# Kernel optimization log

Hardware: AMD Instinct MI355X
Metric: run time of the kernel (lower is better)

Reference implementation:

```python
import jax, jax.numpy as jnp
import numpy as np

B, Ng, C, H, W, Nt, M, P = 4, 8192, 256, 128, 128, 512, 8, 4
Ch = C // M  # 32 channels per head
EPS = 1e-5


def setup_inputs():
    key = jax.random.key(0)
    ks = jax.random.split(key, 12)
    s = 0.02
    def w(k, shape):
        return jax.random.normal(k, shape, jnp.float32) * s
    return {
        "query": jax.random.normal(ks[0], (B, Ng, C), jnp.float32),
        "value": jax.random.normal(ks[1], (B, C, H, W), jnp.float32),
        "reference_points": jax.random.uniform(ks[2], (B, Ng, 2), dtype=jnp.float32),
        "trajectory_points": jax.random.uniform(ks[3], (B, Nt, 2), dtype=jnp.float32),
        "in_proj_w": w(ks[4], (3 * C, C)),
        "in_proj_b": jnp.zeros((3 * C,), jnp.float32),
        "mha_out_w": w(ks[5], (C, C)),
        "mha_out_b": jnp.zeros((C,), jnp.float32),
        "ln_g": jnp.ones((C,), jnp.float32),
        "ln_b": jnp.zeros((C,), jnp.float32),
        "traj_w": w(ks[6], (C, 2)),
        "traj_b": jnp.zeros((C,), jnp.float32),
        "offs_w": w(ks[7], (M * P * 2, C)),
        "offs_b": jnp.zeros((M * P * 2,), jnp.float32),
        "attw_w": w(ks[8], (M * P, C)),
        "attw_b": jnp.zeros((M * P,), jnp.float32),
        "out_w": w(ks[9], (C, C)),
        "out_b": jnp.zeros((C,), jnp.float32),
    }


def _bilinear_sample(imgf, x, y):
    # imgf: (NM, Ch, H*W); x, y: (NM, Lq, P) unnormalized pixel coords
    # grid_sample semantics: bilinear, padding_mode='zeros', align_corners=False
    NM = imgf.shape[0]
    Lq, Pp = x.shape[1], x.shape[2]
    x0 = jnp.floor(x); y0 = jnp.floor(y)
    x1 = x0 + 1.0;     y1 = y0 + 1.0

    def gather(xi, yi):
        valid = (xi >= 0) & (xi < W) & (yi >= 0) & (yi < H)
        xc = jnp.clip(xi, 0, W - 1).astype(jnp.int32)
        yc = jnp.clip(yi, 0, H - 1).astype(jnp.int32)
        idx = (yc * W + xc).reshape(NM, 1, Lq * Pp)
        v = jnp.take_along_axis(imgf, jnp.broadcast_to(idx, (NM, Ch, Lq * Pp)), axis=2)
        return v.reshape(NM, Ch, Lq, Pp), valid.astype(imgf.dtype)

    v00, m00 = gather(x0, y0)
    v01, m01 = gather(x1, y0)
    v10, m10 = gather(x0, y1)
    v11, m11 = gather(x1, y1)
    wx1 = x - x0; wx0 = 1.0 - wx1
    wy1 = y - y0; wy0 = 1.0 - wy1
    out = (v00 * (wx0 * wy0 * m00)[:, None]
         + v01 * (wx1 * wy0 * m01)[:, None]
         + v10 * (wx0 * wy1 * m10)[:, None]
         + v11 * (wx1 * wy1 * m11)[:, None])
    return out  # (NM, Ch, Lq, P)


def reference(query, value, reference_points, trajectory_points,
              in_proj_w, in_proj_b, mha_out_w, mha_out_b, ln_g, ln_b,
              traj_w, traj_b, offs_w, offs_b, attw_w, attw_b, out_w, out_b):
    # trajectory projection: (B,Nt,2) -> (B,Nt,C)
    tf = trajectory_points @ traj_w.T + traj_b

    # guidance cross-attention (nn.MultiheadAttention, eval mode => no dropout)
    wq, wk, wv = jnp.split(in_proj_w, 3, axis=0)
    bq, bk, bv = jnp.split(in_proj_b, 3, axis=0)
    q = (query @ wq.T + bq).reshape(B, Ng, M, Ch)
    k = (tf @ wk.T + bk).reshape(B, Nt, M, Ch)
    v = (tf @ wv.T + bv).reshape(B, Nt, M, Ch)
    scores = jnp.einsum('bqmc,bkmc->bmqk', q, k) / jnp.sqrt(jnp.float32(Ch))
    probs = jax.nn.softmax(scores, axis=-1)
    ctx = jnp.einsum('bmqk,bkmc->bqmc', probs, v).reshape(B, Ng, C)
    ctx = ctx @ mha_out_w.T + mha_out_b

    # residual + LayerNorm
    x = query + ctx
    mu = x.mean(-1, keepdims=True)
    var = ((x - mu) ** 2).mean(-1, keepdims=True)
    gq = (x - mu) / jnp.sqrt(var + EPS) * ln_g + ln_b

    # sampling offsets & softmax attention weights (L=1 level)
    offs = (gq @ offs_w.T + offs_b).reshape(B, Ng, M, 1, P, 2)
    aw = jax.nn.softmax((gq @ attw_w.T + attw_b).reshape(B, Ng, M, P), axis=-1)
    loc = reference_points[:, :, None, None, None, :] + offs  # (B,Ng,M,1,P,2)

    # deformable sampling core (single level)
    grid = 2.0 * loc[:, :, :, 0] - 1.0                   # (B,Ng,M,P,2)
    grid = grid.transpose(0, 2, 1, 3, 4).reshape(B * M, Ng, P, 2)
    gx = (grid[..., 0] + 1.0) * (W * 0.5) - 0.5
    gy = (grid[..., 1] + 1.0) * (H * 0.5) - 0.5
    imgf = value.reshape(B * M, Ch, H * W)               # per-head feature maps
    samp = _bilinear_sample(imgf, gx, gy)                # (B*M,Ch,Ng,P)
    w_att = aw.transpose(0, 2, 1, 3).reshape(B * M, 1, Ng, P)
    out = (samp * w_att).sum(-1)                         # (B*M,Ch,Ng)

    # faithful to source: view(B,M,Ch,Ng).transpose(1,2).contiguous().view(B,Ng,C)
    out = out.reshape(B, M, Ch, Ng).transpose(0, 2, 1, 3).reshape(B, Ng, C)
    return out @ out_w.T + out_b
```

## Files before the change

kernel.cpp:

```cpp
#include <hip/hip_runtime.h>
#include <hip/hip_bf16.h>
#include <stdint.h>

typedef __bf16 bf16_t;
typedef __bf16 bf16x8 __attribute__((ext_vector_type(8)));
typedef __bf16 bf16x4 __attribute__((ext_vector_type(4)));
typedef float f32x4 __attribute__((ext_vector_type(4)));

#define CEXP 0.25506807186679906f

__device__ __forceinline__ float ldf(const void* p, size_t i, int isf) {
  return isf ? ((const float*)p)[i] : (float)((const bf16_t*)p)[i];
}

__device__ __forceinline__ int detect_isf(const void* q) {
  const uint16_t* u = (const uint16_t*)q;
  const int lane = threadIdx.x & 63;
  const uint16_t v = u[2 * lane];
  const int e = (v >> 7) & 0xFF;
  const int weird = (e >= 0x86 || (v != 0 && e <= 0x65)) ? 1 : 0;
  return (__popcll(__ballot(weird)) >= 16) ? 1 : 0;
}

__device__ __forceinline__ float fexp2(float x) {
#if __has_builtin(__builtin_amdgcn_exp2f)
  return __builtin_amdgcn_exp2f(x);
#else
  return exp2f(x);
#endif
}

__device__ __forceinline__ f32x4 mfma16x16x16(bf16x4 a, bf16x4 b, f32x4 c) {
#if __has_builtin(__builtin_amdgcn_mfma_f32_16x16x16_bf16)
  return __builtin_amdgcn_mfma_f32_16x16x16_bf16(a, b, c, 0, 0, 0);
#else
  typedef short s16x4 __attribute__((ext_vector_type(4)));
  return __builtin_amdgcn_mfma_f32_16x16x16bf16_1k(
      __builtin_bit_cast(s16x4, a), __builtin_bit_cast(s16x4, b), c, 0, 0, 0);
#endif
}

__device__ __forceinline__ void stage16(const bf16_t* g, bf16_t* l) {
  __builtin_amdgcn_global_load_lds((const __attribute__((address_space(1))) void*)g,
                                   (__attribute__((address_space(3))) void*)l, 16, 0, 0);
}

__global__ __launch_bounds__(256) void prep_all(
    const void* __restrict__ query,
    const void* in_w, const void* in_b, const void* mow, const void* mob,
    const void* outw, const void* outb,
    const void* trajp, const void* tw, const void* tb,
    const void* offs_w, const void* attw_w, const void* offs_b, const void* attw_b,
    bf16_t* __restrict__ blob, bf16_t* __restrict__ tf,
    bf16_t* __restrict__ Wph, bf16_t* __restrict__ Wpl, bf16_t* __restrict__ bp)
{
  const int isf = detect_isf(query);
  const int bid = blockIdx.x;
  if (bid < 322) {
    const int g = (bid * 256 + threadIdx.x) * 4;
    if (g >= 328960) return;
    const void* src; size_t off;
    if      (g < 196608) { src = in_w; off = g; }
    else if (g < 197376) { src = in_b; off = g - 196608; }
    else if (g < 262912) { src = mow;  off = g - 197376; }
    else if (g < 263168) { src = mob;  off = g - 262912; }
    else if (g < 328704) { src = outw; off = g - 263168; }
    else                 { src = outb; off = g - 328704; }
#pragma unroll
    for (int k = 0; k < 4; k++) blob[g + k] = (bf16_t)ldf(src, off + k, isf);
  } else if (bid < 322 + 2048) {
    const int rowb = bid - 322;
    const int c = threadIdx.x;
    const float x = ldf(trajp, rowb * 2 + 0, isf);
    const float y = ldf(trajp, rowb * 2 + 1, isf);
    const float v = x * ldf(tw, c * 2 + 0, isf) + y * ldf(tw, c * 2 + 1, isf) + ldf(tb, c, isf);
    tf[(size_t)rowb * 256 + c] = (bf16_t)v;
  } else {
    const int idx = (bid - 2370) * 256 + threadIdx.x;
    const int rowp = idx >> 8, c = idx & 255;
    float v = 0.0f;
    if (rowp < 64)      v = ldf(offs_w, rowp * 256 + c, isf);
    else if (rowp < 96) v = ldf(attw_w, (rowp - 64) * 256 + c, isf);
    const bf16_t hi = (bf16_t)v;
    Wph[idx] = hi;
    Wpl[idx] = (bf16_t)(v - (float)hi);
    if (idx < 128) {
      float bv = 0.0f;
      if (idx < 64)      bv = ldf(offs_b, idx, isf);
      else if (idx < 96) bv = ldf(attw_b, idx - 64, isf);
      bp[idx] = (bf16_t)bv;
    }
  }
}

#define TM 128
#define TN 128
#define TKK 64

__global__ __launch_bounds__(256) void gemm_async(
    const bf16_t* __restrict__ A, const bf16_t* __restrict__ W,
    const bf16_t* __restrict__ bias, void* __restrict__ Cout,
    void* __restrict__ Cout2, int Ndim, int Kdim, int mode, float kscale,
    const void* __restrict__ qdet)
{
  __shared__ __align__(16) bf16_t As[TM * TKK];
  __shared__ __align__(16) bf16_t Ws[TN * TKK];
  const int t    = threadIdx.x;
  const int lane = t & 63;
  const int w    = t >> 6;
  const int wm   = (w & 1) * 64;
  const int wn   = (w >> 1) * 64;
  const int q4   = lane >> 4;
  const int r16  = lane & 15;
  const int tm   = blockIdx.x * TM;
  const int tn   = blockIdx.y * TN;

  f32x4 acc[4][4] = {};

  for (int kt = 0; kt < Kdim; kt += TKK) {
    __syncthreads();
#pragma unroll
    for (int r = 0; r < 4; r++) {
      const int L = w * 256 + r * 64 + lane;
      const int R = L >> 3, c = (L & 7) * 8;
      stage16(A + (size_t)(tm + R) * Kdim + kt + c, As + L * 8);
      stage16(W + (size_t)(tn + R) * Kdim + kt + c, Ws + L * 8);
    }
    __syncthreads();
#pragma unroll
    for (int ks = 0; ks < TKK; ks += 32) {
      bf16x8 af[4], bfm[4];
#pragma unroll
      for (int i = 0; i < 4; i++)
        af[i] = *(const bf16x8*)(As + (wm + 16 * i + r16) * TKK + ks + q4 * 8);
#pragma unroll
      for (int j = 0; j < 4; j++)
        bfm[j] = *(const bf16x8*)(Ws + (wn + 16 * j + r16) * TKK + ks + q4 * 8);
#pragma unroll
      for (int i = 0; i < 4; i++)
#pragma unroll
        for (int j = 0; j < 4; j++)
          acc[i][j] = __builtin_amdgcn_mfma_f32_16x16x32_bf16(af[i], bfm[j], acc[i][j], 0, 0, 0);
    }
  }

  const int isf = (mode == 3) ? detect_isf(qdet) : 1;
#pragma unroll
  for (int j = 0; j < 4; j++) {
    const int col = tn + wn + 16 * j + r16;
    const float bv = (float)bias[col];
#pragma unroll
    for (int i = 0; i < 4; i++) {
      const int row0 = tm + wm + 16 * i + q4 * 4;
#pragma unroll
      for (int rr = 0; rr < 4; rr++) {
        const float v = acc[i][j][rr] + bv;
        const size_t off = (size_t)(row0 + rr) * Ndim + col;
        if (mode == 0) {
          ((bf16_t*)Cout)[off] = (bf16_t)v;
        } else if (mode == 6) {
          const int rowg = row0 + rr;
          if (col < 256) {
            ((bf16_t*)Cout)[(size_t)rowg * 256 + col] = (bf16_t)(v * kscale);
          } else {
            const int bb = rowg >> 9, tt = rowg & 511;
            const int c2 = col - 256;
            const int mm = c2 >> 5, ch = c2 & 31;
            ((bf16_t*)Cout2)[(((size_t)(bb * 8 + mm) * 32 + ch) << 9) + tt] = (bf16_t)v;
          }
        } else {
          if (isf) ((float*)Cout)[off] = v; else ((bf16_t*)Cout)[off] = (bf16_t)v;
        }
      }
    }
  }
}

__global__ __launch_bounds__(256) void gemm_f32a(
    const void* __restrict__ Araw, const bf16_t* __restrict__ W,
    const bf16_t* __restrict__ bias, bf16_t* __restrict__ Cout,
    int Ndim, int Kdim, const void* __restrict__ qdet)
{
  __shared__ __align__(16) bf16_t As[TM * TKK];
  __shared__ __align__(16) bf16_t Ws[TN * TKK];
  const int t    = threadIdx.x;
  const int lane = t & 63;
  const int w    = t >> 6;
  const int wm   = (w & 1) * 64;
  const int wn   = (w >> 1) * 64;
  const int q4   = lane >> 4;
  const int r16  = lane & 15;
  const int tm   = blockIdx.x * TM;
  const int tn   = blockIdx.y * TN;
  const int aisf = detect_isf(qdet);

  f32x4 acc[4][4] = {};
  const int srow = t >> 1;
  const int skb  = (t & 1) * 32;

  for (int kt = 0; kt < Kdim; kt += TKK) {
    __syncthreads();
    if (aisf) {
      const float4* ga = (const float4*)((const float*)Araw + (size_t)(tm + srow) * Kdim + kt + skb);
#pragma unroll
      for (int kk = 0; kk < 8; kk++) {
        const float4 u = ga[kk];
        bf16x4 h = {(bf16_t)u.x, (bf16_t)u.y, (bf16_t)u.z, (bf16_t)u.w};
        *(bf16x4*)(As + srow * TKK + skb + kk * 4) = h;
      }
    } else {
      const uint4* ga = (const uint4*)((const bf16_t*)Araw + (size_t)(tm + srow) * Kdim + kt + skb);
      uint4* la = (uint4*)(As + srow * TKK + skb);
      la[0] = ga[0]; la[1] = ga[1]; la[2] = ga[2]; la[3] = ga[3];
    }
    {
      const uint4* gw = (const uint4*)(W + (size_t)(tn + srow) * Kdim + kt + skb);
      uint4* lw = (uint4*)(Ws + srow * TKK + skb);
      lw[0] = gw[0]; lw[1] = gw[1]; lw[2] = gw[2]; lw[3] = gw[3];
    }
    __syncthreads();
#pragma unroll
    for (int ks = 0; ks < TKK; ks += 32) {
      bf16x8 af[4], bfm[4];
#pragma unroll
      for (int i = 0; i < 4; i++)
        af[i] = *(const bf16x8*)(As + (wm + 16 * i + r16) * TKK + ks + q4 * 8);
#pragma unroll
      for (int j = 0; j < 4; j++)
        bfm[j] = *(const bf16x8*)(Ws + (wn + 16 * j + r16) * TKK + ks + q4 * 8);
#pragma unroll
      for (int i = 0; i < 4; i++)
#pragma unroll
        for (int j = 0; j < 4; j++)
          acc[i][j] = __builtin_amdgcn_mfma_f32_16x16x32_bf16(af[i], bfm[j], acc[i][j], 0, 0, 0);
    }
  }

#pragma unroll
  for (int j = 0; j < 4; j++) {
    const int col = tn + wn + 16 * j + r16;
    const float bv = (float)bias[col];
#pragma unroll
    for (int i = 0; i < 4; i++) {
      const int row0 = tm + wm + 16 * i + q4 * 4;
#pragma unroll
      for (int rr = 0; rr < 4; rr++)
        Cout[(size_t)(row0 + rr) * Ndim + col] = (bf16_t)(acc[i][j][rr] + bv);
    }
  }
}

__global__ __launch_bounds__(256, 2) void attn_kernel(
    const bf16_t* __restrict__ Q, const bf16_t* __restrict__ Kk,
    const bf16_t* __restrict__ Vt, bf16_t* __restrict__ ctx)
{
  const int t = threadIdx.x;
  const int lane = t & 63, w = t >> 6;
  const int q4 = lane >> 4, r16 = lane & 15;
  const int bm = blockIdx.y;
  const int b = bm >> 3, m = bm & 7;
  const int q0 = blockIdx.x * 512 + w * 128;

  bf16x8 qf[8];
#pragma unroll
  for (int qt = 0; qt < 8; qt++)
    qf[qt] = *(const bf16x8*)(Q + ((size_t)(b * 8192 + q0 + qt * 16 + r16) * 256 + m * 32 + q4 * 8));

  f32x4 acc[8][2] = {};
  float lsum[8] = {0.f, 0.f, 0.f, 0.f, 0.f, 0.f, 0.f, 0.f};

  const bf16_t* kbase  = Kk + (size_t)b * 512 * 256 + m * 32 + (size_t)r16 * 256 + q4 * 8;
  const bf16_t* vbase0 = Vt + (size_t)bm * 32 * 512 + ((size_t)r16 << 9) + q4 * 4;
  const bf16_t* vbase1 = vbase0 + (16 << 9);

  bf16x8 kfA = *(const bf16x8*)(kbase);
  bf16x4 v0A = *(const bf16x4*)(vbase0);
  bf16x4 v1A = *(const bf16x4*)(vbase1);
  bf16x8 kfB = *(const bf16x8*)(kbase + (size_t)16 * 256);
  bf16x4 v0B = *(const bf16x4*)(vbase0 + 16);
  bf16x4 v1B = *(const bf16x4*)(vbase1 + 16);

  for (int k0 = 0; k0 < 512; k0 += 32) {
    const bf16x8 ka = kfA;
    const bf16x4 va0 = v0A, va1 = v1A;
    kfA = *(const bf16x8*)(kbase + (size_t)(k0 + 32) * 256);
    v0A = *(const bf16x4*)(vbase0 + k0 + 32);
    v1A = *(const bf16x4*)(vbase1 + k0 + 32);
    __builtin_amdgcn_s_setprio(1);
#pragma unroll
    for (int qt = 0; qt < 8; qt++) {
      f32x4 z = {};
      const f32x4 s = __builtin_amdgcn_mfma_f32_16x16x32_bf16(ka, qf[qt], z, 0, 0, 0);
      const float e0 = fexp2(s[0]), e1 = fexp2(s[1]);
      const float e2 = fexp2(s[2]), e3 = fexp2(s[3]);
      lsum[qt] += (e0 + e1) + (e2 + e3);
      const bf16x4 p = {(bf16_t)e0, (bf16_t)e1, (bf16_t)e2, (bf16_t)e3};
      acc[qt][0] = mfma16x16x16(va0, p, acc[qt][0]);
      acc[qt][1] = mfma16x16x16(va1, p, acc[qt][1]);
    }
    __builtin_amdgcn_s_setprio(0);
    const bf16x8 kb = kfB;
    const bf16x4 vb0 = v0B, vb1 = v1B;
    kfB = *(const bf16x8*)(kbase + (size_t)(k0 + 48) * 256);
    v0B = *(const bf16x4*)(vbase0 + k0 + 48);
    v1B = *(const bf16x4*)(vbase1 + k0 + 48);
    __builtin_amdgcn_s_setprio(1);
#pragma unroll
    for (int qt = 0; qt < 8; qt++) {
      f32x4 z = {};
      const f32x4 s = __builtin_amdgcn_mfma_f32_16x16x32_bf16(kb, qf[qt], z, 0, 0, 0);
      const float e0 = fexp2(s[0]), e1 = fexp2(s[1]);
      const float e2 = fexp2(s[2]), e3 = fexp2(s[3]);
      lsum[qt] += (e0 + e1) + (e2 + e3);
      const bf16x4 p = {(bf16_t)e0, (bf16_t)e1, (bf16_t)e2, (bf16_t)e3};
      acc[qt][0] = mfma16x16x16(vb0, p, acc[qt][0]);
      acc[qt][1] = mfma16x16x16(vb1, p, acc[qt][1]);
    }
    __builtin_amdgcn_s_setprio(0);
  }

#pragma unroll
  for (int qt = 0; qt < 8; qt++) {
    float v = lsum[qt];
    v += __shfl_xor(v, 16, 64);
    v += __shfl_xor(v, 32, 64);
    const float inv = 1.0f / v;
    const size_t row = (size_t)b * 8192 + q0 + qt * 16 + r16;
    bf16x4 o0, o1;
#pragma unroll
    for (int rr = 0; rr < 4; rr++) {
      o0[rr] = (bf16_t)(acc[qt][0][rr] * inv);
      o1[rr] = (bf16_t)(acc[qt][1][rr] * inv);
    }
    *(bf16x4*)(ctx + row * 256 + m * 32 + q4 * 4)      = o0;
    *(bf16x4*)(ctx + row * 256 + m * 32 + 16 + q4 * 4) = o1;
  }
}

__global__ __launch_bounds__(256) void ln_kernel(
    const bf16_t* __restrict__ y2, const void* __restrict__ query,
    const void* __restrict__ g, const void* __restrict__ beta,
    bf16_t* __restrict__ gqh, bf16_t* __restrict__ gql)
{
  const int isf = detect_isf(query);
  const int rowb = blockIdx.x * 4 + (threadIdx.x >> 6);
  const int lane = threadIdx.x & 63;
  const size_t base = (size_t)rowb * 256;
  const int c0 = lane * 4;
  float x[4];
  {
    const bf16x4 yv = *(const bf16x4*)(y2 + base + c0);
    if (isf) {
      const float4 qv = *(const float4*)((const float*)query + base + c0);
      x[0] = qv.x + (float)yv[0]; x[1] = qv.y + (float)yv[1];
      x[2] = qv.z + (float)yv[2]; x[3] = qv.w + (float)yv[3];
    } else {
      const bf16x4 qv = *(const bf16x4*)((const bf16_t*)query + base + c0);
#pragma unroll
      for (int k = 0; k < 4; k++) x[k] = (float)qv[k] + (float)yv[k];
    }
  }
  float s = x[0] + x[1] + x[2] + x[3];
  for (int d = 1; d < 64; d <<= 1) s += __shfl_xor(s, d, 64);
  const float mu = s * (1.0f / 256.0f);
  float vs = 0.f;
#pragma unroll
  for (int k = 0; k < 4; k++) { const float d = x[k] - mu; vs += d * d; }
  for (int d = 1; d < 64; d <<= 1) vs += __shfl_xor(vs, d, 64);
  const float rstd = rsqrtf(vs * (1.0f / 256.0f) + 1e-5f);
  float gw[4], bb[4];
  if (isf) {
    const float4 gg = *(const float4*)((const float*)g + c0);
    const float4 bv = *(const float4*)((const float*)beta + c0);
    gw[0] = gg.x; gw[1] = gg.y; gw[2] = gg.z; gw[3] = gg.w;
    bb[0] = bv.x; bb[1] = bv.y; bb[2] = bv.z; bb[3] = bv.w;
  } else {
    const bf16x4 gg = *(const bf16x4*)((const bf16_t*)g + c0);
    const bf16x4 bv = *(const bf16x4*)((const bf16_t*)beta + c0);
#pragma unroll
    for (int k = 0; k < 4; k++) { gw[k] = (float)gg[k]; bb[k] = (float)bv[k]; }
  }
  bf16x4 hi4, lo4;
#pragma unroll
  for (int k = 0; k < 4; k++) {
    const float gv = (x[k] - mu) * rstd * gw[k] + bb[k];
    const bf16_t hi = (bf16_t)gv;
    hi4[k] = hi;
    lo4[k] = (bf16_t)(gv - (float)hi);
  }
  *(bf16x4*)(gqh + base + c0) = hi4;
  *(bf16x4*)(gql + base + c0) = lo4;
}

__global__ __launch_bounds__(256) void gemm_offs(
    const bf16_t* __restrict__ Ahg, const bf16_t* __restrict__ Alg,
    const bf16_t* __restrict__ Whg, const bf16_t* __restrict__ Wlg,
    const bf16_t* __restrict__ bias, float* __restrict__ Cout)
{
  __shared__ __align__(16) bf16_t Ah[128 * 64];
  __shared__ __align__(16) bf16_t Al[128 * 64];
  __shared__ __align__(16) bf16_t Wh[128 * 64];
  __shared__ __align__(16) bf16_t Wl[128 * 64];
  const int t    = threadIdx.x;
  const int lane = t & 63;
  const int w    = t >> 6;
  const int wm   = (w & 1) * 64;
  const int wn   = (w >> 1) * 64;
  const int q4   = lane >> 4;
  const int r16  = lane & 15;
  const int tm   = blockIdx.x * 128;

  f32x4 acc[4][4] = {};
  const int srow = t >> 1;
  const int skb  = (t & 1) * 32;

  for (int kt = 0; kt < 256; kt += 64) {
    __syncthreads();
    {
      const uint4* g0 = (const uint4*)(Ahg + (size_t)(tm + srow) * 256 + kt + skb);
      uint4* l0 = (uint4*)(Ah + srow * 64 + skb);
      l0[0] = g0[0]; l0[1] = g0[1]; l0[2] = g0[2]; l0[3] = g0[3];
      const uint4* g1 = (const uint4*)(Alg + (size_t)(tm + srow) * 256 + kt + skb);
      uint4* l1 = (uint4*)(Al + srow * 64 + skb);
      l1[0] = g1[0]; l1[1] = g1[1]; l1[2] = g1[2]; l1[3] = g1[3];
      const uint4* g2 = (const uint4*)(Whg + (size_t)srow * 256 + kt + skb);
      uint4* l2 = (uint4*)(Wh + srow * 64 + skb);
      l2[0] = g2[0]; l2[1] = g2[1]; l2[2] = g2[2]; l2[3] = g2[3];
      const uint4* g3 = (const uint4*)(Wlg + (size_t)srow * 256 + kt + skb);
      uint4* l3 = (uint4*)(Wl + srow * 64 + skb);
      l3[0] = g3[0]; l3[1] = g3[1]; l3[2] = g3[2]; l3[3] = g3[3];
    }
    __syncthreads();
#pragma unroll
    for (int ks = 0; ks < 64; ks += 32) {
      bf16x8 ah[4], al[4], bh[4], bl[4];
#pragma unroll
      for (int i = 0; i < 4; i++) {
        ah[i] = *(const bf16x8*)(Ah + (wm + 16 * i + r16) * 64 + ks + q4 * 8);
        al[i] = *(const bf16x8*)(Al + (wm + 16 * i + r16) * 64 + ks + q4 * 8);
      }
#pragma unroll
      for (int j = 0; j < 4; j++) {
        bh[j] = *(const bf16x8*)(Wh + (wn + 16 * j + r16) * 64 + ks + q4 * 8);
        bl[j] = *(const bf16x8*)(Wl + (wn + 16 * j + r16) * 64 + ks + q4 * 8);
      }
#pragma unroll
      for (int i = 0; i < 4; i++)
#pragma unroll
        for (int j = 0; j < 4; j++) {
          f32x4 a = acc[i][j];
          a = __builtin_amdgcn_mfma_f32_16x16x32_bf16(al[i], bh[j], a, 0, 0, 0);
          a = __builtin_amdgcn_mfma_f32_16x16x32_bf16(ah[i], bl[j], a, 0, 0, 0);
          a = __builtin_amdgcn_mfma_f32_16x16x32_bf16(ah[i], bh[j], a, 0, 0, 0);
          acc[i][j] = a;
        }
    }
  }

#pragma unroll
  for (int j = 0; j < 4; j++) {
    const int col = wn + 16 * j + r16;
    const float bv = (float)bias[col];
    const int live  = (col < 96) ? 1 : 0;
    const int moff  = (col < 64) ? (col >> 3) : ((col - 64) >> 2);
    const int inner = (col < 64) ? (col & 7) : (8 + (col & 3));
#pragma unroll
    for (int i = 0; i < 4; i++) {
      const int row0 = tm + wm + 16 * i + q4 * 4;
#pragma unroll
      for (int rr = 0; rr < 4; rr++) {
        if (live) {
          const int row = row0 + rr;
          const int bq = row >> 13, q = row & 8191;
          Cout[(((size_t)(bq * 8 + moff) << 13) + q) * 16 + inner] = acc[i][j][rr] + bv;
        }
      }
    }
  }
}

__global__ __launch_bounds__(256) void transpose_value(
    const void* __restrict__ V, bf16_t* __restrict__ Vp, const void* __restrict__ qdet)
{
  __shared__ __align__(16) bf16_t tile[32][136];
  const int isf = detect_isf(qdet);
  const int bid = blockIdx.x;
  const int h = bid & 127;
  const int bm = bid >> 7;
  const int b = bm >> 3, mm = bm & 7;
  const int t = threadIdx.x;
  const int ch  = t >> 3;
  const int ww0 = (t & 7) * 16;
  const size_t ibase = (((size_t)b * 256 + mm * 32 + ch) * 128 + h) * 128 + ww0;
  if (isf) {
    const float4* src = (const float4*)((const float*)V + ibase);
    bf16x8 h0, h1;
#pragma unroll
    for (int k = 0; k < 2; k++) {
      const float4 u0 = src[k * 2], u1 = src[k * 2 + 1];
      bf16x8 hh = {(bf16_t)u0.x, (bf16_t)u0.y, (bf16_t)u0.z, (bf16_t)u0.w,
                   (bf16_t)u1.x, (bf16_t)u1.y, (bf16_t)u1.z, (bf16_t)u1.w};
      if (k == 0) h0 = hh; else h1 = hh;
    }
    *(bf16x8*)(&tile[ch][ww0])     = h0;
    *(bf16x8*)(&tile[ch][ww0 + 8]) = h1;
  } else {
    const bf16x8* src = (const bf16x8*)((const bf16_t*)V + ibase);
    *(bf16x8*)(&tile[ch][ww0])     = src[0];
    *(bf16x8*)(&tile[ch][ww0 + 8]) = src[1];
  }
  __syncthreads();
  const size_t base = ((size_t)bm * 128 + h) * 4096;
  const int ww = t >> 1;
  const int c0 = (t & 1) * 16;
  bf16x8 o0, o1;
#pragma unroll
  for (int e = 0; e < 8; e++) { o0[e] = tile[c0 + e][ww]; o1[e] = tile[c0 + 8 + e][ww]; }
  *(bf16x8*)(Vp + base + ww * 32 + c0)     = o0;
  *(bf16x8*)(Vp + base + ww * 32 + c0 + 8) = o1;
}

__global__ __launch_bounds__(256) void sampler(
    const float* __restrict__ ys2, const void* __restrict__ refp,
    const bf16_t* __restrict__ vperm, bf16_t* __restrict__ outs,
    const void* __restrict__ qdet)
{
  const int isf = detect_isf(qdet);
  const int t = threadIdx.x;
  const int wg = blockIdx.x;
  const int bm  = (wg & 7) + ((wg >> 9) << 3);
  const int mid = (wg >> 3) & 63;
  const int qt  = mid >> 1;
  const int hf  = mid & 1;
  const int b = bm >> 3, m = bm & 7;
  const int qq = qt * 256 + t;
  const size_t row = (size_t)b * 8192 + qq;
  const float* y16 = ys2 + (((size_t)bm << 13) + qq) * 16;
  const float rx = ldf(refp, row * 2 + 0, isf);
  const float ry = ldf(refp, row * 2 + 1, isf);

  const float4 off01 = *(const float4*)(y16 + 0);
  const float4 off23 = *(const float4*)(y16 + 4);
  const float4 lg    = *(const float4*)(y16 + 8);

  const float mx = fmaxf(fmaxf(lg.x, lg.y), fmaxf(lg.z, lg.w));
  const float e0 = __expf(lg.x - mx), e1 = __expf(lg.y - mx);
  const float e2 = __expf(lg.z - mx), e3 = __expf(lg.w - mx);
  const float inv = 1.0f / (e0 + e1 + e2 + e3);
  const float aw[4] = {e0 * inv, e1 * inv, e2 * inv, e3 * inv};
  const float ox[4] = {off01.x, off01.z, off23.x, off23.z};
  const float oy[4] = {off01.y, off01.w, off23.y, off23.w};

  float acc[16];
#pragma unroll
  for (int ch = 0; ch < 16; ch++) acc[ch] = 0.0f;

  const bf16_t* vbase = vperm + (size_t)bm * (128 * 128 * 32) + hf * 16;

  for (int p = 0; p < 4; p++) {
    const float gx = (rx + ox[p]) * 128.0f - 0.5f;
    const float gy = (ry + oy[p]) * 128.0f - 0.5f;
    const float x0f = floorf(gx), y0f = floorf(gy);
    const int x0 = (int)x0f, y0i = (int)y0f;
    const float wx1 = gx - x0f, wx0 = 1.0f - wx1;
    const float wy1 = gy - y0f, wy0 = 1.0f - wy1;
    const float a = aw[p];
    for (int cy = 0; cy < 2; cy++) {
      const int yy = y0i + cy;
      if (yy < 0 || yy >= 128) continue;
      const float wy = cy ? wy1 : wy0;
      for (int cx = 0; cx < 2; cx++) {
        const int xx = x0 + cx;
        if (xx < 0 || xx >= 128) continue;
        const float wgt = a * wy * (cx ? wx1 : wx0);
        const bf16x8* src8 = (const bf16x8*)(vbase + ((size_t)yy * 128 + xx) * 32);
        const bf16x8 d0 = src8[0];
        const bf16x8 d1 = src8[1];
#pragma unroll
        for (int e = 0; e < 8; e++) {
          acc[e]     += wgt * (float)d0[e];
          acc[8 + e] += wgt * (float)d1[e];
        }
      }
    }
  }

  const size_t obase = (size_t)b * 8192;
#pragma unroll
  for (int ch = 0; ch < 16; ch++) {
    const int chg = hf * 16 + ch;
    const size_t orow = obase + (size_t)(chg * 8 + m) * 32 + qt;
    outs[orow * 256 + t] = (bf16_t)acc[ch];
  }
}

extern "C" void kernel_launch(void* const* d_in, const int* in_sizes, int n_in,
                              void* d_out, int out_size, void* d_ws, size_t ws_size,
                              hipStream_t stream) {
  const void* query = d_in[0];
  const void* value = d_in[1];
  const void* refp  = d_in[2];
  const void* trajp = d_in[3];
  const void* in_w  = d_in[4];
  const void* in_b  = d_in[5];
  const void* mow   = d_in[6];
  const void* mob   = d_in[7];
  const void* lng   = d_in[8];
  const void* lnb   = d_in[9];
  const void* tw    = d_in[10];
  const void* tb    = d_in[11];
  const void* ow    = d_in[12];
  const void* ob    = d_in[13];
  const void* aww   = d_in[14];
  const void* awb   = d_in[15];
  const void* outw  = d_in[16];
  const void* outb  = d_in[17];

  char* base = (char*)d_ws;
  float*  ysamp = (float*)(base);
  bf16_t* qout  = (bf16_t*)(base + 16777216);
  bf16_t* ctx   = (bf16_t*)(base + 33554432);
  bf16_t* y2    = (bf16_t*)(base + 50331648);
  bf16_t* tf_ws = (bf16_t*)(base + 67108864);
  bf16_t* k_ws  = (bf16_t*)(base + 68157440);
  bf16_t* vt_g  = (bf16_t*)(base + 69206016);
  bf16_t* blob  = (bf16_t*)(base + 70254592);

  bf16_t* gqh   = qout;
  bf16_t* gql   = ctx;
  bf16_t* vperm = (bf16_t*)(base + 16777216);
  bf16_t* outs  = y2;

  bf16_t* inw_bf  = blob;
  bf16_t* inb_bf  = blob + 196608;
  bf16_t* mow_bf  = blob + 197376;
  bf16_t* mob_bf  = blob + 262912;
  bf16_t* outw_bf = blob + 263168;
  bf16_t* outb_bf = blob + 328704;
  bf16_t* wph     = blob + 328960;
  bf16_t* wpl     = blob + 361728;
  bf16_t* bpad    = blob + 394496;

  prep_all<<<dim3(2498), dim3(256), 0, stream>>>(
      query, in_w, in_b, mow, mob, outw, outb, trajp, tw, tb,
      ow, aww, ob, awb, blob, tf_ws, wph, wpl, bpad);
  gemm_async<<<dim3(16, 4), dim3(256), 0, stream>>>(
      tf_ws, inw_bf + 65536, inb_bf + 256, (void*)k_ws, (void*)vt_g, 512, 256, 6, CEXP, query);
  gemm_f32a<<<dim3(256, 2), dim3(256), 0, stream>>>(
      query, inw_bf, inb_bf, qout, 256, 256, query);
  attn_kernel<<<dim3(16, 32), dim3(256), 0, stream>>>(qout, k_ws, vt_g, ctx);
  gemm_async<<<dim3(256, 2), dim3(256), 0, stream>>>(
      ctx, mow_bf, mob_bf, (void*)y2, nullptr, 256, 256, 0, 1.0f, query);
  ln_kernel<<<dim3(8192), dim3(256), 0, stream>>>(y2, query, lng, lnb, gqh, gql);
  gemm_offs<<<dim3(256, 1), dim3(256), 0, stream>>>(gqh, gql, wph, wpl, bpad, ysamp);
  transpose_value<<<dim3(4096), dim3(256), 0, stream>>>(value, vperm, query);
  sampler<<<dim3(2048), dim3(256), 0, stream>>>(ysamp, refp, vperm, outs, query);
  gemm_async<<<dim3(256, 2), dim3(256), 0, stream>>>(
      outs, outw_bf, outb_bf, d_out, nullptr, 256, 256, 3, 1.0f, query);
}
```

Measured before the change: 336.3 us.

## Fuse value transpose into prep kernel and merge Q and KV projections

Moves the value-tensor transpose/bf16 conversion out of its own launch and into the prep_all kernel as extra blocks. Vperm gets its own workspace region so it no longer aliases qout. The separate Q projection and K/V projection GEMMs become one gemm_qkv launch that dispatches on block index. This removes two kernel launches and lets independent work share one grid, at the cost of a larger prep grid and a bigger workspace footprint.

```diff
diff --git a/kernel.cpp b/kernel.cpp
--- a/kernel.cpp
+++ b/kernel.cpp
@@ -52,8 +52,10 @@
     const void* trajp, const void* tw, const void* tb,
     const void* offs_w, const void* attw_w, const void* offs_b, const void* attw_b,
     bf16_t* __restrict__ blob, bf16_t* __restrict__ tf,
-    bf16_t* __restrict__ Wph, bf16_t* __restrict__ Wpl, bf16_t* __restrict__ bp)
+    bf16_t* __restrict__ Wph, bf16_t* __restrict__ Wpl, bf16_t* __restrict__ bp,
+    const void* __restrict__ V, bf16_t* __restrict__ Vp)
 {
+  __shared__ __align__(16) bf16_t tile[32][136];
   const int isf = detect_isf(query);
   const int bid = blockIdx.x;
   if (bid < 322) {
@@ -75,7 +77,7 @@
     const float y = ldf(trajp, rowb * 2 + 1, isf);
     const float v = x * ldf(tw, c * 2 + 0, isf) + y * ldf(tw, c * 2 + 1, isf) + ldf(tb, c, isf);
     tf[(size_t)rowb * 256 + c] = (bf16_t)v;
-  } else {
+  } else if (bid < 2498) {
     const int idx = (bid - 2370) * 256 + threadIdx.x;
     const int rowp = idx >> 8, c = idx & 255;
     float v = 0.0f;
@@ -90,6 +92,41 @@
       else if (idx < 96) bv = ldf(attw_b, idx - 64, isf);
       bp[idx] = (bf16_t)bv;
     }
+  } else {
+    const int vb = bid - 2498;
+    const int h = vb & 127;
+    const int bm = vb >> 7;
+    const int b = bm >> 3, mm = bm & 7;
+    const int t = threadIdx.x;
+    const int ch  = t >> 3;
+    const int ww0 = (t & 7) * 16;
+    const size_t ibase = (((size_t)b * 256 + mm * 32 + ch) * 128 + h) * 128 + ww0;
+    if (isf) {
+      const float4* src = (const float4*)((const float*)V + ibase);
+      bf16x8 h0, h1;
+#pragma unroll
+      for (int k = 0; k < 2; k++) {
+        const float4 u0 = src[k * 2], u1 = src[k * 2 + 1];
+        bf16x8 hh = {(bf16_t)u0.x, (bf16_t)u0.y, (bf16_t)u0.z, (bf16_t)u0.w,
+                     (bf16_t)u1.x, (bf16_t)u1.y, (bf16_t)u1.z, (bf16_t)u1.w};
+        if (k == 0) h0 = hh; else h1 = hh;
+      }
+      *(bf16x8*)(&tile[ch][ww0])     = h0;
+      *(bf16x8*)(&tile[ch][ww0 + 8]) = h1;
+    } else {
+      const bf16x8* src = (const bf16x8*)((const bf16_t*)V + ibase);
+      *(bf16x8*)(&tile[ch][ww0])     = src[0];
+      *(bf16x8*)(&tile[ch][ww0 + 8]) = src[1];
+    }
+    __syncthreads();
+    const size_t base = ((size_t)bm * 128 + h) * 4096;
+    const int ww = t >> 1;
+    const int c0 = (t & 1) * 16;
+    bf16x8 o0, o1;
+#pragma unroll
+    for (int e = 0; e < 8; e++) { o0[e] = tile[c0 + e][ww]; o1[e] = tile[c0 + 8 + e][ww]; }
+    *(bf16x8*)(Vp + base + ww * 32 + c0)     = o0;
+    *(bf16x8*)(Vp + base + ww * 32 + c0 + 8) = o1;
   }
 }
 
@@ -158,16 +195,6 @@
         const size_t off = (size_t)(row0 + rr) * Ndim + col;
         if (mode == 0) {
           ((bf16_t*)Cout)[off] = (bf16_t)v;
-        } else if (mode == 6) {
-          const int rowg = row0 + rr;
-          if (col < 256) {
-            ((bf16_t*)Cout)[(size_t)rowg * 256 + col] = (bf16_t)(v * kscale);
-          } else {
-            const int bb = rowg >> 9, tt = rowg & 511;
-            const int c2 = col - 256;
-            const int mm = c2 >> 5, ch = c2 & 31;
-            ((bf16_t*)Cout2)[(((size_t)(bb * 8 + mm) * 32 + ch) << 9) + tt] = (bf16_t)v;
-          }
         } else {
           if (isf) ((float*)Cout)[off] = v; else ((bf16_t*)Cout)[off] = (bf16_t)v;
         }
@@ -176,10 +203,12 @@
   }
 }
 
-__global__ __launch_bounds__(256) void gemm_f32a(
-    const void* __restrict__ Araw, const bf16_t* __restrict__ W,
-    const bf16_t* __restrict__ bias, bf16_t* __restrict__ Cout,
-    int Ndim, int Kdim, const void* __restrict__ qdet)
+__global__ __launch_bounds__(256) void gemm_qkv(
+    const void* __restrict__ Araw, const bf16_t* __restrict__ Wq,
+    const bf16_t* __restrict__ bq, bf16_t* __restrict__ Cq,
+    const bf16_t* __restrict__ Atf, const bf16_t* __restrict__ Wkv,
+    const bf16_t* __restrict__ bkv, bf16_t* __restrict__ Kout,
+    bf16_t* __restrict__ Vtout, float kscale, const void* __restrict__ qdet)
 {
   __shared__ __align__(16) bf16_t As[TM * TKK];
   __shared__ __align__(16) bf16_t Ws[TN * TKK];
@@ -190,62 +219,120 @@
   const int wn   = (w >> 1) * 64;
   const int q4   = lane >> 4;
   const int r16  = lane & 15;
-  const int tm   = blockIdx.x * TM;
-  const int tn   = blockIdx.y * TN;
-  const int aisf = detect_isf(qdet);
+  const int blk  = blockIdx.x;
 
   f32x4 acc[4][4] = {};
-  const int srow = t >> 1;
-  const int skb  = (t & 1) * 32;
-
-  for (int kt = 0; kt < Kdim; kt += TKK) {
-    __syncthreads();
-    if (aisf) {
-      const float4* ga = (const float4*)((const float*)Araw + (size_t)(tm + srow) * Kdim + kt + skb);
-#pragma unroll
-      for (int kk = 0; kk < 8; kk++) {
-        const float4 u = ga[kk];
-        bf16x4 h = {(bf16_t)u.x, (bf16_t)u.y, (bf16_t)u.z, (bf16_t)u.w};
-        *(bf16x4*)(As + srow * TKK + skb + kk * 4) = h;
-      }
-    } else {
-      const uint4* ga = (const uint4*)((const bf16_t*)Araw + (size_t)(tm + srow) * Kdim + kt + skb);
-      uint4* la = (uint4*)(As + srow * TKK + skb);
-      la[0] = ga[0]; la[1] = ga[1]; la[2] = ga[2]; la[3] = ga[3];
-    }
-    {
-      const uint4* gw = (const uint4*)(W + (size_t)(tn + srow) * Kdim + kt + skb);
-      uint4* lw = (uint4*)(Ws + srow * TKK + skb);
-      lw[0] = gw[0]; lw[1] = gw[1]; lw[2] = gw[2]; lw[3] = gw[3];
-    }
-    __syncthreads();
-#pragma unroll
-    for (int ks = 0; ks < TKK; ks += 32) {
-      bf16x8 af[4], bfm[4];
-#pragma unroll
-      for (int i = 0; i < 4; i++)
-        af[i] = *(const bf16x8*)(As + (wm + 16 * i + r16) * TKK + ks + q4 * 8);
-#pragma unroll
-      for (int j = 0; j < 4; j++)
-        bfm[j] = *(const bf16x8*)(Ws + (wn + 16 * j + r16) * TKK + ks + q4 * 8);
-#pragma unroll
-      for (int i = 0; i < 4; i++)
+
+  if (blk < 512) {
+    const int tm = (blk >> 1) * TM;
+    const int tn = (blk & 1) * TN;
+    const int aisf = detect_isf(qdet);
+    const int srow = t >> 1;
+    const int skb  = (t & 1) * 32;
+
+    for (int kt = 0; kt < 256; kt += TKK) {
+      __syncthreads();
+      if (aisf) {
+        const float4* ga = (const float4*)((const float*)Araw + (size_t)(tm + srow) * 256 + kt + skb);
+#pragma unroll
+        for (int kk = 0; kk < 8; kk++) {
+          const float4 u = ga[kk];
+          bf16x4 h = {(bf16_t)u.x, (bf16_t)u.y, (bf16_t)u.z, (bf16_t)u.w};
+          *(bf16x4*)(As + srow * TKK + skb + kk * 4) = h;
+        }
+      } else {
+        const uint4* ga = (const uint4*)((const bf16_t*)Araw + (size_t)(tm + srow) * 256 + kt + skb);
+        uint4* la = (uint4*)(As + srow * TKK + skb);
+        la[0] = ga[0]; la[1] = ga[1]; la[2] = ga[2]; la[3] = ga[3];
+      }
+      {
+        const uint4* gw = (const uint4*)(Wq + (size_t)(tn + srow) * 256 + kt + skb);
+        uint4* lw = (uint4*)(Ws + srow * TKK + skb);
+        lw[0] = gw[0]; lw[1] = gw[1]; lw[2] = gw[2]; lw[3] = gw[3];
+      }
+      __syncthreads();
+#pragma unroll
+      for (int ks = 0; ks < TKK; ks += 32) {
+        bf16x8 af[4], bfm[4];
+#pragma unroll
+        for (int i = 0; i < 4; i++)
+          af[i] = *(const bf16x8*)(As + (wm + 16 * i + r16) * TKK + ks + q4 * 8);
 #pragma unroll
         for (int j = 0; j < 4; j++)
-          acc[i][j] = __builtin_amdgcn_mfma_f32_16x16x32_bf16(af[i], bfm[j], acc[i][j], 0, 0, 0);
-    }
-  }
-
-#pragma unroll
-  for (int j = 0; j < 4; j++) {
-    const int col = tn + wn + 16 * j + r16;
-    const float bv = (float)bias[col];
-#pragma unroll
-    for (int i = 0; i < 4; i++) {
-      const int row0 = tm + wm + 16 * i + q4 * 4;
-#pragma unroll
-      for (int rr = 0; rr < 4; rr++)
-        Cout[(size_t)(row0 + rr) * Ndim + col] = (bf16_t)(acc[i][j][rr] + bv);
+          bfm[j] = *(const bf16x8*)(Ws + (wn + 16 * j + r16) * TKK + ks + q4 * 8);
+#pragma unroll
+        for (int i = 0; i < 4; i++)
+#pragma unroll
+          for (int j = 0; j < 4; j++)
+            acc[i][j] = __builtin_amdgcn_mfma_f32_16x16x32_bf16(af[i], bfm[j], acc[i][j], 0, 0, 0);
+      }
+    }
+
+#pragma unroll
+    for (int j = 0; j < 4; j++) {
+      const int col = tn + wn + 16 * j + r16;
+      const float bv = (float)bq[col];
+#pragma unroll
+      for (int i = 0; i < 4; i++) {
+        const int row0 = tm + wm + 16 * i + q4 * 4;
+#pragma unroll
+        for (int rr = 0; rr < 4; rr++)
+          Cq[(size_t)(row0 + rr) * 256 + col] = (bf16_t)(acc[i][j][rr] + bv);
+      }
+    }
+  } else {
+    const int k = blk - 512;
+    const int tm = (k & 15) * TM;
+    const int tn = (k >> 4) * TN;
+
+    for (int kt = 0; kt < 256; kt += TKK) {
+      __syncthreads();
+#pragma unroll
+      for (int r = 0; r < 4; r++) {
+        const int L = w * 256 + r * 64 + lane;
+        const int R = L >> 3, c = (L & 7) * 8;
+        stage16(Atf + (size_t)(tm + R) * 256 + kt + c, As + L * 8);
+        stage16(Wkv + (size_t)(tn + R) * 256 + kt + c, Ws + L * 8);
+      }
+      __syncthreads();
+#pragma unroll
+      for (int ks = 0; ks < TKK; ks += 32) {
+        bf16x8 af[4], bfm[4];
+#pragma unroll
+        for (int i = 0; i < 4; i++)
+          af[i] = *(const bf16x8*)(As + (wm + 16 * i + r16) * TKK + ks + q4 * 8);
+#pragma unroll
+        for (int j = 0; j < 4; j++)
+          bfm[j] = *(const bf16x8*)(Ws + (wn + 16 * j + r16) * TKK + ks + q4 * 8);
+#pragma unroll
+        for (int i = 0; i < 4; i++)
+#pragma unroll
+          for (int j = 0; j < 4; j++)
+            acc[i][j] = __builtin_amdgcn_mfma_f32_16x16x32_bf16(af[i], bfm[j], acc[i][j], 0, 0, 0);
+      }
+    }
+
+#pragma unroll
+    for (int j = 0; j < 4; j++) {
+      const int col = tn + wn + 16 * j + r16;
+      const float bv = (float)bkv[col];
+#pragma unroll
+      for (int i = 0; i < 4; i++) {
+        const int row0 = tm + wm + 16 * i + q4 * 4;
+#pragma unroll
+        for (int rr = 0; rr < 4; rr++) {
+          const float v = acc[i][j][rr] + bv;
+          const int rowg = row0 + rr;
+          if (col < 256) {
+            Kout[(size_t)rowg * 256 + col] = (bf16_t)(v * kscale);
+          } else {
+            const int bb = rowg >> 9, tt = rowg & 511;
+            const int c2 = col - 256;
+            const int mm = c2 >> 5, ch = c2 & 31;
+            Vtout[(((size_t)(bb * 8 + mm) * 32 + ch) << 9) + tt] = (bf16_t)v;
+          }
+        }
+      }
     }
   }
 }
@@ -477,47 +564,6 @@
       }
     }
   }
-}
-
-__global__ __launch_bounds__(256) void transpose_value(
-    const void* __restrict__ V, bf16_t* __restrict__ Vp, const void* __restrict__ qdet)
-{
-  __shared__ __align__(16) bf16_t tile[32][136];
-  const int isf = detect_isf(qdet);
-  const int bid = blockIdx.x;
-  const int h = bid & 127;
-  const int bm = bid >> 7;
-  const int b = bm >> 3, mm = bm & 7;
-  const int t = threadIdx.x;
-  const int ch  = t >> 3;
-  const int ww0 = (t & 7) * 16;
-  const size_t ibase = (((size_t)b * 256 + mm * 32 + ch) * 128 + h) * 128 + ww0;
-  if (isf) {
-    const float4* src = (const float4*)((const float*)V + ibase);
-    bf16x8 h0, h1;
-#pragma unroll
-    for (int k = 0; k < 2; k++) {
-      const float4 u0 = src[k * 2], u1 = src[k * 2 + 1];
-      bf16x8 hh = {(bf16_t)u0.x, (bf16_t)u0.y, (bf16_t)u0.z, (bf16_t)u0.w,
-                   (bf16_t)u1.x, (bf16_t)u1.y, (bf16_t)u1.z, (bf16_t)u1.w};
-      if (k == 0) h0 = hh; else h1 = hh;
-    }
-    *(bf16x8*)(&tile[ch][ww0])     = h0;
-    *(bf16x8*)(&tile[ch][ww0 + 8]) = h1;
-  } else {
-    const bf16x8* src = (const bf16x8*)((const bf16_t*)V + ibase);
-    *(bf16x8*)(&tile[ch][ww0])     = src[0];
-    *(bf16x8*)(&tile[ch][ww0 + 8]) = src[1];
-  }
-  __syncthreads();
-  const size_t base = ((size_t)bm * 128 + h) * 4096;
-  const int ww = t >> 1;
-  const int c0 = (t & 1) * 16;
-  bf16x8 o0, o1;
-#pragma unroll
-  for (int e = 0; e < 8; e++) { o0[e] = tile[c0 + e][ww]; o1[e] = tile[c0 + 8 + e][ww]; }
-  *(bf16x8*)(Vp + base + ww * 32 + c0)     = o0;
-  *(bf16x8*)(Vp + base + ww * 32 + c0 + 8) = o1;
 }
 
 __global__ __launch_bounds__(256) void sampler(
@@ -628,7 +674,7 @@
 
   bf16_t* gqh   = qout;
   bf16_t* gql   = ctx;
-  bf16_t* vperm = (bf16_t*)(base + 16777216);
+  bf16_t* vperm = (bf16_t*)(base + 134217728);
   bf16_t* outs  = y2;
 
   bf16_t* inw_bf  = blob;
@@ -641,19 +687,17 @@
   bf16_t* wpl     = blob + 361728;
   bf16_t* bpad    = blob + 394496;
 
-  prep_all<<<dim3(2498), dim3(256), 0, stream>>>(
+  prep_all<<<dim3(6594), dim3(256), 0, stream>>>(
       query, in_w, in_b, mow, mob, outw, outb, trajp, tw, tb,
-      ow, aww, ob, awb, blob, tf_ws, wph, wpl, bpad);
-  gemm_async<<<dim3(16, 4), dim3(256), 0, stream>>>(
-      tf_ws, inw_bf + 65536, inb_bf + 256, (void*)k_ws, (void*)vt_g, 512, 256, 6, CEXP, query);
-  gemm_f32a<<<dim3(256, 2), dim3(256), 0, stream>>>(
-      query, inw_bf, inb_bf, qout, 256, 256, query);
+      ow, aww, ob, awb, blob, tf_ws, wph, wpl, bpad, value, vperm);
+  gemm_qkv<<<dim3(576), dim3(256), 0, stream>>>(
+      query, inw_bf, inb_bf, qout,
+      tf_ws, inw_bf + 65536, inb_bf + 256, k_ws, vt_g, CEXP, query);
   attn_kernel<<<dim3(16, 32), dim3(256), 0, stream>>>(qout, k_ws, vt_g, ctx);
   gemm_async<<<dim3(256, 2), dim3(256), 0, stream>>>(
       ctx, mow_bf, mob_bf, (void*)y2, nullptr, 256, 256, 0, 1.0f, query);
   ln_kernel<<<dim3(8192), dim3(256), 0, stream>>>(y2, query, lng, lnb, gqh, gql);
   gemm_offs<<<dim3(256, 1), dim3(256), 0, stream>>>(gqh, gql, wph, wpl, bpad, ysamp);
-  transpose_value<<<dim3(4096), dim3(256), 0, stream>>>(value, vperm, query);
   sampler<<<dim3(2048), dim3(256), 0, stream>>>(ysamp, refp, vperm, outs, query);
   gemm_async<<<dim3(256, 2), dim3(256), 0, stream>>>(
       outs, outw_bf, outb_bf, d_out, nullptr, 256, 256, 3, 1.0f, query);
```

Measured after the change: 333.5 us. About the same (-0.8%).
